# Kernel optimization log

Hardware: AMD Instinct MI355X
Metric: run time of the kernel (lower is better)

Reference implementation:

```python
import jax, jax.numpy as jnp
import numpy as np

BS, NC, C, D = 8, 64, 256, 32
K, KB, ALPHA, B = 16, 8, 4, 16
HS, HM, HMOD = 64, 64, 32
N = NC * C
DLM = NC * D
MOD_IN = K + 3 * D + 1    # 113
MOD_OUT = K + KB + 1 + D  # 57


def setup_inputs() -> dict:
    key = jax.random.key(0)
    ks = jax.random.split(key, 12)
    rn = lambda k, s, sc=1.0: jax.random.normal(k, s, dtype=jnp.float32) * sc
    s_in, m_in = 3 * D + 1, 3 * D
    inp = {}
    inp['cc_signals_t'] = rn(ks[0], (BS, DLM))
    inp['h'] = rn(ks[1], (BS, NC, C, D), 0.1)
    inp['prev_messages'] = rn(ks[2], (BS, NC, C, D), 0.1)
    inp['decay_logit'] = jnp.zeros((BS, NC, C), jnp.float32)
    inp['primitives_state'] = jnp.zeros((BS, NC, C, D), jnp.float32)
    inp['hebbian_traces'] = jnp.zeros((BS, NC, C, K), jnp.float32)
    inp['state_w1'] = rn(ks[3], (HS, s_in), (2.0 / (s_in + HS)) ** 0.5)
    inp['state_b1'] = jnp.zeros((HS,), jnp.float32)
    inp['state_w2'] = rn(ks[4], (D, HS), (2.0 / (HS + D)) ** 0.5)
    inp['state_b2'] = jnp.zeros((D,), jnp.float32)
    inp['msg_w1'] = rn(ks[5], (HM, m_in), (2.0 / (m_in + HM)) ** 0.5)
    inp['msg_b1'] = jnp.zeros((HM,), jnp.float32)
    inp['msg_w2'] = rn(ks[6], (D, HM), (2.0 / (HM + D)) ** 0.5)
    inp['msg_b2'] = jnp.zeros((D,), jnp.float32)
    inp['mod_w1'] = rn(ks[7], (N, HMOD, MOD_IN), (2.0 / (MOD_IN + HMOD)) ** 0.5)
    inp['mod_b1'] = jnp.zeros((N, HMOD), jnp.float32)
    inp['mod_w2'] = rn(ks[8], (N, HMOD, MOD_OUT), (2.0 / (HMOD + MOD_OUT)) ** 0.5)
    inp['mod_b2'] = jnp.zeros((N, MOD_OUT), jnp.float32)
    inp['neuron_id'] = rn(ks[9], (NC, C, D), 1.0 / D ** 0.5)
    inp['conn_indices'] = jax.random.randint(ks[10], (NC, C, K), 0, C)
    inp['border_conn_indices'] = jax.random.randint(ks[11], (NC, B, KB), 0, NC * B)
    return inp


def reference(cc_signals_t, h, prev_messages, decay_logit, primitives_state,
              hebbian_traces, state_w1, state_b1, state_w2, state_b2,
              msg_w1, msg_b1, msg_w2, msg_b2,
              mod_w1, mod_b1, mod_w2, mod_b2, neuron_id,
              conn_indices, border_conn_indices):
    # ---- per-neuron modulator: each of N=NC*C neurons has unique MLP weights ----
    nid = jnp.broadcast_to(neuron_id[None], (BS, NC, C, D))
    mod_inp = jnp.concatenate(
        [hebbian_traces, h, decay_logit[..., None], primitives_state, nid], axis=-1)
    flat = mod_inp.reshape(BS, N, MOD_IN)
    hid = jnp.tanh(jnp.einsum('bni,nhi->bnh', flat, mod_w1) + mod_b1)
    out = (jnp.einsum('bnh,nho->bno', hid, mod_w2) + mod_b2).reshape(BS, NC, C, MOD_OUT)
    new_w_conn = out[..., :K]                          # [BS,NC,C,K]
    w_border = out[:, :, ALPHA:ALPHA + B, K:K + KB]    # border neurons only [BS,NC,B,KB]
    new_decay = out[..., K + KB]                       # [BS,NC,C]
    new_prim = out[..., K + KB + 1:]                   # [BS,NC,C,D]

    # ---- intra-cell weighted neighbor gather (irregular gather) ----
    cell = jnp.arange(NC)[:, None, None]
    neighbor = prev_messages[:, cell, conn_indices]    # [BS,NC,C,K,D]
    received = jnp.einsum('bnckd,bnck->bncd', neighbor, jax.nn.sigmoid(new_w_conn))

    # ---- inter-cell border gather over global border neuron pool ----
    border_msgs = prev_messages[:, :, ALPHA:ALPHA + B, :].reshape(BS, NC * B, D)
    nb = border_msgs[:, border_conn_indices]           # [BS,NC,B,KB,D]
    recv_border = jnp.einsum('bnjkd,bnjk->bnjd', nb, jax.nn.sigmoid(w_border))
    received = received.at[:, :, ALPHA:ALPHA + B, :].add(recv_border)

    # ---- inject external signal into the first ALPHA neurons of each cell ----
    inj = cc_signals_t.reshape(BS, NC, 1, D)
    received = received.at[:, :, :ALPHA, :].add(
        jnp.broadcast_to(inj, (BS, NC, ALPHA, D)))

    # ---- decay-gated state update through shared state MLP ----
    primitives_new = primitives_state + new_prim
    decay = jax.nn.sigmoid(new_decay)[..., None]       # [BS,NC,C,1]
    s_in = jnp.concatenate([h, received, primitives_new, decay], axis=-1)  # 3D+1
    sh = jnp.tanh(jnp.einsum('...i,hi->...h', s_in, state_w1) + state_b1)
    dh = jnp.einsum('...h,dh->...d', sh, state_w2) + state_b2
    h_new = decay * h + (1.0 - decay) * jnp.tanh(dh)

    # ---- shared message MLP ----
    m_in = jnp.concatenate([h_new, received, nid], axis=-1)  # 3D
    mh = jnp.tanh(jnp.einsum('...i,hi->...h', m_in, msg_w1) + msg_b1)
    msg = jnp.tanh(jnp.einsum('...h,dh->...d', mh, msg_w2) + msg_b2)

    # ---- hebbian trace EMA: pre/post message correlation per connection ----
    nb_new = msg[:, cell, conn_indices]                # [BS,NC,C,K,D]
    corr = jnp.einsum('bncd,bnckd->bnck', msg, nb_new) / D
    hebbian_new = 0.9 * hebbian_traces + 0.1 * corr

    # ---- readout: mean over last ALPHA (readout) neurons per cell ----
    readout = msg[:, :, C - ALPHA:, :].mean(axis=2).reshape(BS, DLM)
    return readout, h_new, msg, hebbian_new
```

## Files before the change

### kernel.cpp

```cpp
#include <hip/hip_runtime.h>
#include <cstdint>
#include <cstddef>

constexpr int kBS = 8;
constexpr int kNC = 64;
constexpr int kC = 256;
constexpr int kD = 32;
constexpr int kK = 16;
constexpr int kKB = 8;
constexpr int kALPHA = 4;
constexpr int kB = 16;
constexpr int kHS = 64;
constexpr int kHM = 64;
constexpr int kHMOD = 32;
constexpr int kN = kNC * kC;
constexpr int kMODIN = kK + 3 * kD + 1;
constexpr int kMODOUT = kK + kKB + 1 + kD;
constexpr int kXS = 116;
constexpr int kW1S = 100;
constexpr int kSLAB = 36;

constexpr size_t kO1 = (size_t)kBS * kNC * kD;
constexpr size_t kO2 = kO1 + (size_t)kBS * kN * kD;
constexpr size_t kO3 = kO2 + (size_t)kBS * kN * kD;

__device__ __forceinline__ float sigmoidf_(float x) {
    return 1.0f / (1.0f + __expf(-x));
}
__device__ __forceinline__ float rdlane(float v, int l) {
    return __int_as_float(__builtin_amdgcn_readlane(__float_as_int(v), l));
}

__global__ __launch_bounds__(256) void mod_mlp_kernel(
    const float* __restrict__ heb, const float* __restrict__ h,
    const float* __restrict__ dlog, const float* __restrict__ prim,
    const float* __restrict__ nid,
    const float* __restrict__ mw1, const float* __restrict__ mb1,
    const float* __restrict__ mw2, const float* __restrict__ mb2,
    float* __restrict__ modout, int mos, int poff)
{
    const int wv = threadIdx.x >> 6;
    const int lane = threadIdx.x & 63;
    const int n = (blockIdx.x << 2) | wv;

    __shared__ __align__(16) float xs[4][kBS * kXS];
    float* xw = xs[wv];

    for (int t = lane; t < kBS * kMODIN; t += 64) {
        int b = t / kMODIN;
        int i = t - b * kMODIN;
        size_t nb = (size_t)b * kN + n;
        float v;
        if (i < kK)                 v = heb[nb * kK + i];
        else if (i < kK + kD)       v = h[nb * kD + (i - kK)];
        else if (i == kK + kD)      v = dlog[nb];
        else if (i < kK + 2*kD + 1) v = prim[nb * kD + (i - (kK + kD + 1))];
        else                        v = nid[(size_t)n * kD + (i - (kK + 2*kD + 1))];
        xw[b * kXS + i] = v;
    }
    __syncthreads();

    const int hh = lane & 31;
    const int bh = lane >> 5;
    const float* wg = mw1 + ((size_t)n * kHMOD + hh) * kMODIN;
    float a0 = 0.f, a1 = 0.f, a2 = 0.f, a3 = 0.f;
    #pragma unroll 4
    for (int q = 0; q < 28; ++q) {
        float w0 = wg[4*q+0], w1 = wg[4*q+1], w2 = wg[4*q+2], w3 = wg[4*q+3];
        const float4 x0 = *(const float4*)(xw + (bh+0) * kXS + 4*q);
        const float4 x1 = *(const float4*)(xw + (bh+2) * kXS + 4*q);
        const float4 x2 = *(const float4*)(xw + (bh+4) * kXS + 4*q);
        const float4 x3 = *(const float4*)(xw + (bh+6) * kXS + 4*q);
        a0 += w0*x0.x + w1*x0.y + w2*x0.z + w3*x0.w;
        a1 += w0*x1.x + w1*x1.y + w2*x1.z + w3*x1.w;
        a2 += w0*x2.x + w1*x2.y + w2*x2.z + w3*x2.w;
        a3 += w0*x3.x + w1*x3.y + w2*x3.z + w3*x3.w;
    }
    {
        float w112 = wg[112];
        a0 += w112 * xw[(bh+0)*kXS + 112];
        a1 += w112 * xw[(bh+2)*kXS + 112];
        a2 += w112 * xw[(bh+4)*kXS + 112];
        a3 += w112 * xw[(bh+6)*kXS + 112];
    }
    const float bb = mb1[(size_t)n * kHMOD + hh];
    float h0 = tanhf(a0 + bb);
    float h1 = tanhf(a1 + bb);
    float h2 = tanhf(a2 + bb);
    float h3 = tanhf(a3 + bb);

    const int o = (lane < kMODOUT) ? lane : (kMODOUT - 1);
    const float* w2g = mw2 + (size_t)n * (kHMOD * kMODOUT);
    float ob0=0.f, ob1=0.f, ob2=0.f, ob3=0.f, ob4=0.f, ob5=0.f, ob6=0.f, ob7=0.f;
    #pragma unroll
    for (int hx = 0; hx < kHMOD; ++hx) {
        float w = w2g[hx * kMODOUT + o];
        ob0 += rdlane(h0, hx)      * w;
        ob1 += rdlane(h0, hx + 32) * w;
        ob2 += rdlane(h1, hx)      * w;
        ob3 += rdlane(h1, hx + 32) * w;
        ob4 += rdlane(h2, hx)      * w;
        ob5 += rdlane(h2, hx + 32) * w;
        ob6 += rdlane(h3, hx)      * w;
        ob7 += rdlane(h3, hx + 32) * w;
    }
    if (lane < kMODOUT) {
        const float bo = mb2[(size_t)n * kMODOUT + o];
        const int oo = (o < 25) ? o : (o + (poff - 25));
        modout[((size_t)0 * kN + n) * mos + oo] = ob0 + bo;
        modout[((size_t)1 * kN + n) * mos + oo] = ob1 + bo;
        modout[((size_t)2 * kN + n) * mos + oo] = ob2 + bo;
        modout[((size_t)3 * kN + n) * mos + oo] = ob3 + bo;
        modout[((size_t)4 * kN + n) * mos + oo] = ob4 + bo;
        modout[((size_t)5 * kN + n) * mos + oo] = ob5 + bo;
        modout[((size_t)6 * kN + n) * mos + oo] = ob6 + bo;
        modout[((size_t)7 * kN + n) * mos + oo] = ob7 + bo;
    }
}

__global__ __launch_bounds__(256) void cell_kernel(
    const float* __restrict__ cc, const float* __restrict__ hin,
    const float* __restrict__ pmsg, const float* __restrict__ prim,
    const float* __restrict__ hebin, const float* __restrict__ nid,
    const float* __restrict__ sw1, const float* __restrict__ sb1,
    const float* __restrict__ sw2, const float* __restrict__ sb2,
    const float* __restrict__ mw1g, const float* __restrict__ mb1g,
    const float* __restrict__ mw2g, const float* __restrict__ mb2g,
    const int* __restrict__ conn, const int* __restrict__ bconn,
    const float* __restrict__ modout, float* __restrict__ out,
    int mos, int poff)
{
    const int nc = blockIdx.x;
    const int b  = blockIdx.y;
    const int c  = threadIdx.x;

    __shared__ __align__(16) float slab[kC * kSLAB];
    __shared__ __align__(16) float w1s[kHS * kW1S];
    __shared__ __align__(16) float w2ts[kHS * kD];
    __shared__ __align__(16) float mw1s[kHM * 96];
    __shared__ __align__(16) float mw2ts[kHM * kD];
    __shared__ float sb1s[kHS], sb2s[kD], mb1s[kHM], mb2s[kD];

    const size_t cellrow = ((size_t)b * kNC + nc) * kC;
    const size_t nbase   = cellrow + c;

    for (int idx = c; idx < kHS * 97; idx += kC) {
        int r = idx / 97, ci = idx - r * 97;
        w1s[r * kW1S + ci] = sw1[idx];
    }
    for (int idx = c; idx < kHM * 96; idx += kC) mw1s[idx] = mw1g[idx];
    for (int idx = c; idx < kHS * kD; idx += kC) {
        int o2 = idx >> 6, h2 = idx & 63;
        w2ts[h2 * kD + o2] = sw2[idx];
    }
    for (int idx = c; idx < kHM * kD; idx += kC) {
        int o2 = idx >> 6, h2 = idx & 63;
        mw2ts[h2 * kD + o2] = mw2g[idx];
    }
    if (c < kHS) sb1s[c] = sb1[c];
    if (c < kD)  sb2s[c] = sb2[c];
    if (c < kHM) mb1s[c] = mb1g[c];
    if (c < kD)  mb2s[c] = mb2g[c];

    {
        const float4* s4 = (const float4*)(pmsg + cellrow * kD);
        for (int i = c; i < (kC * kD) / 4; i += kC) {
            float4 v = s4[i];
            *(float4*)&slab[(i >> 3) * kSLAB + ((i & 7) << 2)] = v;
        }
    }

    float hreg[32];
    {
        const float4* src = (const float4*)(hin + nbase * kD);
        #pragma unroll
        for (int q = 0; q < 8; ++q) {
            float4 v = src[q];
            hreg[4*q] = v.x; hreg[4*q+1] = v.y; hreg[4*q+2] = v.z; hreg[4*q+3] = v.w;
        }
    }
    const float* mo = modout + nbase * mos;
    float wcon[16];
    if (poff == 28) {
        const float4* m4 = (const float4*)mo;
        float4 va = m4[0], vb = m4[1], vc = m4[2], vd = m4[3];
        wcon[0]=sigmoidf_(va.x);  wcon[1]=sigmoidf_(va.y);  wcon[2]=sigmoidf_(va.z);  wcon[3]=sigmoidf_(va.w);
        wcon[4]=sigmoidf_(vb.x);  wcon[5]=sigmoidf_(vb.y);  wcon[6]=sigmoidf_(vb.z);  wcon[7]=sigmoidf_(vb.w);
        wcon[8]=sigmoidf_(vc.x);  wcon[9]=sigmoidf_(vc.y);  wcon[10]=sigmoidf_(vc.z); wcon[11]=sigmoidf_(vc.w);
        wcon[12]=sigmoidf_(vd.x); wcon[13]=sigmoidf_(vd.y); wcon[14]=sigmoidf_(vd.z); wcon[15]=sigmoidf_(vd.w);
    } else {
        #pragma unroll
        for (int k = 0; k < 16; ++k) wcon[k] = sigmoidf_(mo[k]);
    }
    int jreg[16];
    {
        const int4* cr = (const int4*)(conn + ((size_t)nc * kC + c) * kK);
        #pragma unroll
        for (int q = 0; q < 4; ++q) {
            int4 v = cr[q];
            jreg[4*q] = v.x; jreg[4*q+1] = v.y; jreg[4*q+2] = v.z; jreg[4*q+3] = v.w;
        }
    }
    const float decay = sigmoidf_(mo[kK + kKB]);
    float pnew[32];
    {
        const float4* p4 = (const float4*)(prim + nbase * kD);
        if (poff == 28) {
            const float4* d4 = (const float4*)(mo + 28);
            #pragma unroll
            for (int q = 0; q < 8; ++q) {
                float4 v = p4[q], w = d4[q];
                pnew[4*q]   = v.x + w.x;
                pnew[4*q+1] = v.y + w.y;
                pnew[4*q+2] = v.z + w.z;
                pnew[4*q+3] = v.w + w.w;
            }
        } else {
            #pragma unroll
            for (int q = 0; q < 8; ++q) {
                float4 v = p4[q];
                pnew[4*q]   = v.x + mo[25 + 4*q];
                pnew[4*q+1] = v.y + mo[25 + 4*q + 1];
                pnew[4*q+2] = v.z + mo[25 + 4*q + 2];
                pnew[4*q+3] = v.w + mo[25 + 4*q + 3];
            }
        }
    }
    __syncthreads();

    float recv[32];
    #pragma unroll
    for (int d = 0; d < 32; ++d) recv[d] = 0.f;
    #pragma unroll 1
    for (int k = 0; k < 16; ++k) {
        const float4* row = (const float4*)(slab + jreg[k] * kSLAB);
        const float w = wcon[k];
        #pragma unroll
        for (int q = 0; q < 8; ++q) {
            float4 v = row[q];
            recv[4*q]   += v.x * w;
            recv[4*q+1] += v.y * w;
            recv[4*q+2] += v.z * w;
            recv[4*q+3] += v.w * w;
        }
    }
    if (c >= kALPHA && c < kALPHA + kB) {
        const int j = c - kALPHA;
        const int* br = bconn + ((size_t)nc * kB + j) * kKB;
        #pragma unroll 1
        for (int kb = 0; kb < kKB; ++kb) {
            int g = br[kb];
            int nc2 = g >> 4;
            int c2 = kALPHA + (g & 15);
            const float4* src = (const float4*)(pmsg + (((size_t)b * kNC + nc2) * kC + c2) * kD);
            float w = sigmoidf_(mo[kK + kb]);
            #pragma unroll
            for (int q = 0; q < 8; ++q) {
                float4 v = src[q];
                recv[4*q]   += v.x * w;
                recv[4*q+1] += v.y * w;
                recv[4*q+2] += v.z * w;
                recv[4*q+3] += v.w * w;
            }
        }
    }
    if (c < kALPHA) {
        const float* src = cc + (size_t)b * (kNC * kD) + nc * kD;
        #pragma unroll
        for (int d = 0; d < 32; ++d) recv[d] += src[d];
    }

    float dh[32];
    #pragma unroll
    for (int o = 0; o < 32; ++o) dh[o] = sb2s[o];
    #pragma unroll 2
    for (int hh = 0; hh < kHS; ++hh) {
        const float4* w4 = (const float4*)(w1s + hh * kW1S);
        float p0 = 0.f, p1 = 0.f, p2 = 0.f, p3 = 0.f;
        #pragma unroll
        for (int q = 0; q < 8; ++q) {
            float4 wv = w4[q];
            p0 += hreg[4*q] * wv.x;   p1 += hreg[4*q+1] * wv.y;
            p2 += hreg[4*q+2] * wv.z; p3 += hreg[4*q+3] * wv.w;
        }
        #pragma unroll
        for (int q = 0; q < 8; ++q) {
            float4 wv = w4[8+q];
            p0 += recv[4*q] * wv.x;   p1 += recv[4*q+1] * wv.y;
            p2 += recv[4*q+2] * wv.z; p3 += recv[4*q+3] * wv.w;
        }
        #pragma unroll
        for (int q = 0; q < 8; ++q) {
            float4 wv = w4[16+q];
            p0 += pnew[4*q] * wv.x;   p1 += pnew[4*q+1] * wv.y;
            p2 += pnew[4*q+2] * wv.z; p3 += pnew[4*q+3] * wv.w;
        }
        float acc = sb1s[hh] + ((p0 + p1) + (p2 + p3)) + decay * w1s[hh * kW1S + 96];
        const float s = tanhf(acc);
        const float4* w2r = (const float4*)(w2ts + hh * kD);
        #pragma unroll
        for (int q = 0; q < 8; ++q) {
            float4 wv = w2r[q];
            dh[4*q]   += s * wv.x;
            dh[4*q+1] += s * wv.y;
            dh[4*q+2] += s * wv.z;
            dh[4*q+3] += s * wv.w;
        }
    }
    float hnew[32];
    #pragma unroll
    for (int d = 0; d < 32; ++d) hnew[d] = decay * hreg[d] + (1.f - decay) * tanhf(dh[d]);

    {
        float4* dst = (float4*)(out + kO1 + nbase * kD);
        #pragma unroll
        for (int q = 0; q < 8; ++q)
            dst[q] = make_float4(hnew[4*q], hnew[4*q+1], hnew[4*q+2], hnew[4*q+3]);
    }

    float nidr[32];
    {
        const float4* src = (const float4*)(nid + ((size_t)nc * kC + c) * kD);
        #pragma unroll
        for (int q = 0; q < 8; ++q) {
            float4 v = src[q];
            nidr[4*q] = v.x; nidr[4*q+1] = v.y; nidr[4*q+2] = v.z; nidr[4*q+3] = v.w;
        }
    }
    float mm[32];
    #pragma unroll
    for (int o = 0; o < 32; ++o) mm[o] = mb2s[o];
    #pragma unroll 2
    for (int hh = 0; hh < kHM; ++hh) {
        const float4* w4 = (const float4*)(mw1s + hh * 96);
        float p0 = 0.f, p1 = 0.f, p2 = 0.f, p3 = 0.f;
        #pragma unroll
        for (int q = 0; q < 8; ++q) {
            float4 wv = w4[q];
            p0 += hnew[4*q] * wv.x;   p1 += hnew[4*q+1] * wv.y;
            p2 += hnew[4*q+2] * wv.z; p3 += hnew[4*q+3] * wv.w;
        }
        #pragma unroll
        for (int q = 0; q < 8; ++q) {
            float4 wv = w4[8+q];
            p0 += recv[4*q] * wv.x;   p1 += recv[4*q+1] * wv.y;
            p2 += recv[4*q+2] * wv.z; p3 += recv[4*q+3] * wv.w;
        }
        #pragma unroll
        for (int q = 0; q < 8; ++q) {
            float4 wv = w4[16+q];
            p0 += nidr[4*q] * wv.x;   p1 += nidr[4*q+1] * wv.y;
            p2 += nidr[4*q+2] * wv.z; p3 += nidr[4*q+3] * wv.w;
        }
        const float s = tanhf(mb1s[hh] + ((p0 + p1) + (p2 + p3)));
        const float4* w2r = (const float4*)(mw2ts + hh * kD);
        #pragma unroll
        for (int q = 0; q < 8; ++q) {
            float4 wv = w2r[q];
            mm[4*q]   += s * wv.x;
            mm[4*q+1] += s * wv.y;
            mm[4*q+2] += s * wv.z;
            mm[4*q+3] += s * wv.w;
        }
    }
    float msgr[32];
    #pragma unroll
    for (int d = 0; d < 32; ++d) msgr[d] = tanhf(mm[d]);

    __syncthreads();
    {
        float4* row = (float4*)(slab + c * kSLAB);
        #pragma unroll
        for (int q = 0; q < 8; ++q)
            row[q] = make_float4(msgr[4*q], msgr[4*q+1], msgr[4*q+2], msgr[4*q+3]);
    }
    __syncthreads();

    {
        const float* hb = hebin + nbase * kK;
        float* dst = out + kO3 + nbase * kK;
        #pragma unroll 1
        for (int k = 0; k < 16; ++k) {
            const float4* row = (const float4*)(slab + jreg[k] * kSLAB);
            float dot = 0.f;
            #pragma unroll
            for (int q = 0; q < 8; ++q) {
                float4 v = row[q];
                dot += msgr[4*q] * v.x + msgr[4*q+1] * v.y
                     + msgr[4*q+2] * v.z + msgr[4*q+3] * v.w;
            }
            dst[k] = 0.9f * hb[k] + 0.1f * (dot * (1.0f / 32.0f));
        }
    }
    {
        float4* dst = (float4*)(out + kO2 + cellrow * kD);
        for (int i = c; i < (kC * kD) / 4; i += kC)
            dst[i] = *(const float4*)&slab[(i >> 3) * kSLAB + ((i & 7) << 2)];
    }
    if (c < kD) {
        float s = 0.25f * (slab[(kC-4)*kSLAB + c] + slab[(kC-3)*kSLAB + c] +
                           slab[(kC-2)*kSLAB + c] + slab[(kC-1)*kSLAB + c]);
        out[(size_t)b * (kNC * kD) + nc * kD + c] = s;
    }
}

extern "C" void kernel_launch(void* const* d_in, const int* in_sizes, int n_in,
                              void* d_out, int out_size, void* d_ws, size_t ws_size,
                              hipStream_t stream)
{
    const float* cc    = (const float*)d_in[0];
    const float* h     = (const float*)d_in[1];
    const float* pmsg  = (const float*)d_in[2];
    const float* dlog  = (const float*)d_in[3];
    const float* prim  = (const float*)d_in[4];
    const float* heb   = (const float*)d_in[5];
    const float* sw1   = (const float*)d_in[6];
    const float* sb1   = (const float*)d_in[7];
    const float* sw2   = (const float*)d_in[8];
    const float* sb2   = (const float*)d_in[9];
    const float* mw1   = (const float*)d_in[10];
    const float* mb1   = (const float*)d_in[11];
    const float* mw2   = (const float*)d_in[12];
    const float* mb2   = (const float*)d_in[13];
    const float* modw1 = (const float*)d_in[14];
    const float* modb1 = (const float*)d_in[15];
    const float* modw2 = (const float*)d_in[16];
    const float* modb2 = (const float*)d_in[17];
    const float* nid   = (const float*)d_in[18];
    const int*   conn  = (const int*)d_in[19];
    const int*   bconn = (const int*)d_in[20];
    float* out = (float*)d_out;
    float* modout = (float*)d_ws;

    int mos = 57, poff = 25;
    if (ws_size >= (size_t)kBS * kN * 60 * sizeof(float)) { mos = 60; poff = 28; }

    mod_mlp_kernel<<<kN / 4, 256, 0, stream>>>(heb, h, dlog, prim, nid,
                                               modw1, modb1, modw2, modb2,
                                               modout, mos, poff);
    cell_kernel<<<dim3(kNC, kBS), kC, 0, stream>>>(cc, h, pmsg, prim, heb, nid,
                                                   sw1, sb1, sw2, sb2,
                                                   mw1, mb1, mw2, mb2,
                                                   conn, bconn, modout, out,
                                                   mos, poff);
}
```

Before: 766.1 us.

## Restructure mod MLP to one neuron per block; read shared-MLP W1 from global

The per-neuron modulator kernel now gives each neuron a whole 256-thread block. It stages that neuron's W1 and W2 in LDS with coalesced float4 loads, computes the hidden layer one (batch, hidden) pair per thread, and runs the output layer from LDS instead of using cross-lane readlane broadcasts. The cell kernel stops staging the shared state and message W1 matrices and biases in LDS and reads them from global or scalar memory with uniform addresses. It also pads the transposed W2 tiles and removes the vectorized modout loads for the padded layout. This cuts LDS footprint and setup cost, but the mod kernel launches four times as many blocks, and the cell kernel's inner loops now depend on global or constant-cache weight loads.

```diff
diff --git a/kernel.cpp b/kernel.cpp
--- a/kernel.cpp
+++ b/kernel.cpp
@@ -17,8 +17,9 @@
 constexpr int kMODIN = kK + 3 * kD + 1;
 constexpr int kMODOUT = kK + kKB + 1 + kD;
 constexpr int kXS = 116;
-constexpr int kW1S = 100;
+constexpr int kWS = 116;
 constexpr int kSLAB = 36;
+constexpr int kW2TS = 36;
 
 constexpr size_t kO1 = (size_t)kBS * kNC * kD;
 constexpr size_t kO2 = kO1 + (size_t)kBS * kN * kD;
@@ -26,9 +27,6 @@
 
 __device__ __forceinline__ float sigmoidf_(float x) {
     return 1.0f / (1.0f + __expf(-x));
-}
-__device__ __forceinline__ float rdlane(float v, int l) {
-    return __int_as_float(__builtin_amdgcn_readlane(__float_as_int(v), l));
 }
 
 __global__ __launch_bounds__(256) void mod_mlp_kernel(
@@ -39,82 +37,85 @@
     const float* __restrict__ mw2, const float* __restrict__ mb2,
     float* __restrict__ modout, int mos, int poff)
 {
-    const int wv = threadIdx.x >> 6;
-    const int lane = threadIdx.x & 63;
-    const int n = (blockIdx.x << 2) | wv;
-
-    __shared__ __align__(16) float xs[4][kBS * kXS];
-    float* xw = xs[wv];
-
-    for (int t = lane; t < kBS * kMODIN; t += 64) {
-        int b = t / kMODIN;
-        int i = t - b * kMODIN;
-        size_t nb = (size_t)b * kN + n;
-        float v;
-        if (i < kK)                 v = heb[nb * kK + i];
-        else if (i < kK + kD)       v = h[nb * kD + (i - kK)];
-        else if (i == kK + kD)      v = dlog[nb];
-        else if (i < kK + 2*kD + 1) v = prim[nb * kD + (i - (kK + kD + 1))];
-        else                        v = nid[(size_t)n * kD + (i - (kK + 2*kD + 1))];
-        xw[b * kXS + i] = v;
-    }
-    __syncthreads();
-
-    const int hh = lane & 31;
-    const int bh = lane >> 5;
-    const float* wg = mw1 + ((size_t)n * kHMOD + hh) * kMODIN;
-    float a0 = 0.f, a1 = 0.f, a2 = 0.f, a3 = 0.f;
-    #pragma unroll 4
-    for (int q = 0; q < 28; ++q) {
-        float w0 = wg[4*q+0], w1 = wg[4*q+1], w2 = wg[4*q+2], w3 = wg[4*q+3];
-        const float4 x0 = *(const float4*)(xw + (bh+0) * kXS + 4*q);
-        const float4 x1 = *(const float4*)(xw + (bh+2) * kXS + 4*q);
-        const float4 x2 = *(const float4*)(xw + (bh+4) * kXS + 4*q);
-        const float4 x3 = *(const float4*)(xw + (bh+6) * kXS + 4*q);
-        a0 += w0*x0.x + w1*x0.y + w2*x0.z + w3*x0.w;
-        a1 += w0*x1.x + w1*x1.y + w2*x1.z + w3*x1.w;
-        a2 += w0*x2.x + w1*x2.y + w2*x2.z + w3*x2.w;
-        a3 += w0*x3.x + w1*x3.y + w2*x3.z + w3*x3.w;
-    }
-    {
-        float w112 = wg[112];
-        a0 += w112 * xw[(bh+0)*kXS + 112];
-        a1 += w112 * xw[(bh+2)*kXS + 112];
-        a2 += w112 * xw[(bh+4)*kXS + 112];
-        a3 += w112 * xw[(bh+6)*kXS + 112];
-    }
-    const float bb = mb1[(size_t)n * kHMOD + hh];
-    float h0 = tanhf(a0 + bb);
-    float h1 = tanhf(a1 + bb);
-    float h2 = tanhf(a2 + bb);
-    float h3 = tanhf(a3 + bb);
-
-    const int o = (lane < kMODOUT) ? lane : (kMODOUT - 1);
-    const float* w2g = mw2 + (size_t)n * (kHMOD * kMODOUT);
-    float ob0=0.f, ob1=0.f, ob2=0.f, ob3=0.f, ob4=0.f, ob5=0.f, ob6=0.f, ob7=0.f;
-    #pragma unroll
-    for (int hx = 0; hx < kHMOD; ++hx) {
-        float w = w2g[hx * kMODOUT + o];
-        ob0 += rdlane(h0, hx)      * w;
-        ob1 += rdlane(h0, hx + 32) * w;
-        ob2 += rdlane(h1, hx)      * w;
-        ob3 += rdlane(h1, hx + 32) * w;
-        ob4 += rdlane(h2, hx)      * w;
-        ob5 += rdlane(h2, hx + 32) * w;
-        ob6 += rdlane(h3, hx)      * w;
-        ob7 += rdlane(h3, hx + 32) * w;
-    }
-    if (lane < kMODOUT) {
-        const float bo = mb2[(size_t)n * kMODOUT + o];
-        const int oo = (o < 25) ? o : (o + (poff - 25));
-        modout[((size_t)0 * kN + n) * mos + oo] = ob0 + bo;
-        modout[((size_t)1 * kN + n) * mos + oo] = ob1 + bo;
-        modout[((size_t)2 * kN + n) * mos + oo] = ob2 + bo;
-        modout[((size_t)3 * kN + n) * mos + oo] = ob3 + bo;
-        modout[((size_t)4 * kN + n) * mos + oo] = ob4 + bo;
-        modout[((size_t)5 * kN + n) * mos + oo] = ob5 + bo;
-        modout[((size_t)6 * kN + n) * mos + oo] = ob6 + bo;
-        modout[((size_t)7 * kN + n) * mos + oo] = ob7 + bo;
+    const int n = blockIdx.x;
+    const int tid = threadIdx.x;
+
+    __shared__ __align__(16) float xw[kBS * kXS];
+    __shared__ __align__(16) float w1s[kHMOD * kWS];
+    __shared__ __align__(16) float w2s[kHMOD * kMODOUT];
+    __shared__ float hids[kBS * kHMOD];
+
+    {
+        const float4* w1g4 = (const float4*)(mw1 + (size_t)n * (kHMOD * kMODIN));
+        #pragma unroll
+        for (int r = 0; r < 4; ++r) {
+            int t = tid + 256 * r;
+            if (t < (kHMOD * kMODIN) / 4) {
+                float4 v = w1g4[t];
+                int f = t << 2;
+                #pragma unroll
+                for (int e = 0; e < 4; ++e) {
+                    int fe = f + e;
+                    int row = fe / kMODIN;
+                    int col = fe - row * kMODIN;
+                    float val = (e == 0) ? v.x : (e == 1) ? v.y : (e == 2) ? v.z : v.w;
+                    w1s[row * kWS + col] = val;
+                }
+            }
+        }
+    }
+    {
+        const float4* w2g4 = (const float4*)(mw2 + (size_t)n * (kHMOD * kMODOUT));
+        #pragma unroll
+        for (int r = 0; r < 2; ++r) {
+            int t = tid + 256 * r;
+            if (t < (kHMOD * kMODOUT) / 4)
+                *(float4*)&w2s[t << 2] = w2g4[t];
+        }
+    }
+    {
+        if (tid < kBS * kK) {
+            int b = tid >> 4, i = tid & 15;
+            xw[b * kXS + i] = heb[((size_t)b * kN + n) * kK + i];
+        }
+        {
+            int b = tid >> 5, d = tid & 31;
+            xw[b * kXS + 16 + d] = h[((size_t)b * kN + n) * kD + d];
+            xw[b * kXS + 49 + d] = prim[((size_t)b * kN + n) * kD + d];
+            xw[b * kXS + 81 + d] = nid[(size_t)n * kD + d];
+        }
+        if (tid < kBS)
+            xw[tid * kXS + 48] = dlog[(size_t)tid * kN + n];
+    }
+    __syncthreads();
+
+    {
+        const int hh = tid & 31;
+        const int b  = tid >> 5;
+        const float* wr = w1s + hh * kWS;
+        const float* xr = xw + b * kXS;
+        float acc = mb1[(size_t)n * kHMOD + hh];
+        #pragma unroll 4
+        for (int q = 0; q < 28; ++q) {
+            float4 wv = *(const float4*)(wr + 4*q);
+            float4 xv = *(const float4*)(xr + 4*q);
+            acc += wv.x*xv.x + wv.y*xv.y + wv.z*xv.z + wv.w*xv.w;
+        }
+        acc += wr[112] * xr[112];
+        hids[b * kHMOD + hh] = tanhf(acc);
+    }
+    __syncthreads();
+
+    for (int t = tid; t < kBS * kMODOUT; t += 256) {
+        int b2 = t / kMODOUT;
+        int o  = t - b2 * kMODOUT;
+        const float* hr = hids + b2 * kHMOD;
+        float acc = mb2[(size_t)n * kMODOUT + o];
+        #pragma unroll
+        for (int hx = 0; hx < kHMOD; ++hx)
+            acc += hr[hx] * w2s[hx * kMODOUT + o];
+        int oo = (o < 25) ? o : (o + (poff - 25));
+        modout[((size_t)b2 * kN + n) * mos + oo] = acc;
     }
 }
 
@@ -135,32 +136,20 @@
     const int c  = threadIdx.x;
 
     __shared__ __align__(16) float slab[kC * kSLAB];
-    __shared__ __align__(16) float w1s[kHS * kW1S];
-    __shared__ __align__(16) float w2ts[kHS * kD];
-    __shared__ __align__(16) float mw1s[kHM * 96];
-    __shared__ __align__(16) float mw2ts[kHM * kD];
-    __shared__ float sb1s[kHS], sb2s[kD], mb1s[kHM], mb2s[kD];
+    __shared__ __align__(16) float w2ts[kHS * kW2TS];
+    __shared__ __align__(16) float mw2ts[kHM * kW2TS];
 
     const size_t cellrow = ((size_t)b * kNC + nc) * kC;
     const size_t nbase   = cellrow + c;
 
-    for (int idx = c; idx < kHS * 97; idx += kC) {
-        int r = idx / 97, ci = idx - r * 97;
-        w1s[r * kW1S + ci] = sw1[idx];
-    }
-    for (int idx = c; idx < kHM * 96; idx += kC) mw1s[idx] = mw1g[idx];
     for (int idx = c; idx < kHS * kD; idx += kC) {
         int o2 = idx >> 6, h2 = idx & 63;
-        w2ts[h2 * kD + o2] = sw2[idx];
+        w2ts[h2 * kW2TS + o2] = sw2[idx];
     }
     for (int idx = c; idx < kHM * kD; idx += kC) {
         int o2 = idx >> 6, h2 = idx & 63;
-        mw2ts[h2 * kD + o2] = mw2g[idx];
-    }
-    if (c < kHS) sb1s[c] = sb1[c];
-    if (c < kD)  sb2s[c] = sb2[c];
-    if (c < kHM) mb1s[c] = mb1g[c];
-    if (c < kD)  mb2s[c] = mb2g[c];
+        mw2ts[h2 * kW2TS + o2] = mw2g[idx];
+    }
 
     {
         const float4* s4 = (const float4*)(pmsg + cellrow * kD);
@@ -181,17 +170,8 @@
     }
     const float* mo = modout + nbase * mos;
     float wcon[16];
-    if (poff == 28) {
-        const float4* m4 = (const float4*)mo;
-        float4 va = m4[0], vb = m4[1], vc = m4[2], vd = m4[3];
-        wcon[0]=sigmoidf_(va.x);  wcon[1]=sigmoidf_(va.y);  wcon[2]=sigmoidf_(va.z);  wcon[3]=sigmoidf_(va.w);
-        wcon[4]=sigmoidf_(vb.x);  wcon[5]=sigmoidf_(vb.y);  wcon[6]=sigmoidf_(vb.z);  wcon[7]=sigmoidf_(vb.w);
-        wcon[8]=sigmoidf_(vc.x);  wcon[9]=sigmoidf_(vc.y);  wcon[10]=sigmoidf_(vc.z); wcon[11]=sigmoidf_(vc.w);
-        wcon[12]=sigmoidf_(vd.x); wcon[13]=sigmoidf_(vd.y); wcon[14]=sigmoidf_(vd.z); wcon[15]=sigmoidf_(vd.w);
-    } else {
-        #pragma unroll
-        for (int k = 0; k < 16; ++k) wcon[k] = sigmoidf_(mo[k]);
-    }
+    #pragma unroll
+    for (int k = 0; k < 16; ++k) wcon[k] = sigmoidf_(mo[k]);
     int jreg[16];
     {
         const int4* cr = (const int4*)(conn + ((size_t)nc * kC + c) * kK);
@@ -205,25 +185,14 @@
     float pnew[32];
     {
         const float4* p4 = (const float4*)(prim + nbase * kD);
-        if (poff == 28) {
-            const float4* d4 = (const float4*)(mo + 28);
-            #pragma unroll
-            for (int q = 0; q < 8; ++q) {
-                float4 v = p4[q], w = d4[q];
-                pnew[4*q]   = v.x + w.x;
-                pnew[4*q+1] = v.y + w.y;
-                pnew[4*q+2] = v.z + w.z;
-                pnew[4*q+3] = v.w + w.w;
-            }
-        } else {
-            #pragma unroll
-            for (int q = 0; q < 8; ++q) {
-                float4 v = p4[q];
-                pnew[4*q]   = v.x + mo[25 + 4*q];
-                pnew[4*q+1] = v.y + mo[25 + 4*q + 1];
-                pnew[4*q+2] = v.z + mo[25 + 4*q + 2];
-                pnew[4*q+3] = v.w + mo[25 + 4*q + 3];
-            }
+        const int pbase = poff;
+        #pragma unroll
+        for (int q = 0; q < 8; ++q) {
+            float4 v = p4[q];
+            pnew[4*q]   = v.x + mo[pbase + 4*q];
+            pnew[4*q+1] = v.y + mo[pbase + 4*q + 1];
+            pnew[4*q+2] = v.z + mo[pbase + 4*q + 2];
+            pnew[4*q+3] = v.w + mo[pbase + 4*q + 3];
         }
     }
     __syncthreads();
@@ -272,32 +241,19 @@
 
     float dh[32];
     #pragma unroll
-    for (int o = 0; o < 32; ++o) dh[o] = sb2s[o];
+    for (int o = 0; o < 32; ++o) dh[o] = sb2[o];
     #pragma unroll 2
     for (int hh = 0; hh < kHS; ++hh) {
-        const float4* w4 = (const float4*)(w1s + hh * kW1S);
-        float p0 = 0.f, p1 = 0.f, p2 = 0.f, p3 = 0.f;
-        #pragma unroll
-        for (int q = 0; q < 8; ++q) {
-            float4 wv = w4[q];
-            p0 += hreg[4*q] * wv.x;   p1 += hreg[4*q+1] * wv.y;
-            p2 += hreg[4*q+2] * wv.z; p3 += hreg[4*q+3] * wv.w;
-        }
-        #pragma unroll
-        for (int q = 0; q < 8; ++q) {
-            float4 wv = w4[8+q];
-            p0 += recv[4*q] * wv.x;   p1 += recv[4*q+1] * wv.y;
-            p2 += recv[4*q+2] * wv.z; p3 += recv[4*q+3] * wv.w;
-        }
-        #pragma unroll
-        for (int q = 0; q < 8; ++q) {
-            float4 wv = w4[16+q];
-            p0 += pnew[4*q] * wv.x;   p1 += pnew[4*q+1] * wv.y;
-            p2 += pnew[4*q+2] * wv.z; p3 += pnew[4*q+3] * wv.w;
-        }
-        float acc = sb1s[hh] + ((p0 + p1) + (p2 + p3)) + decay * w1s[hh * kW1S + 96];
+        const float* w = sw1 + hh * (3 * kD + 1);
+        float acc = sb1[hh] + decay * w[96];
+        #pragma unroll
+        for (int i = 0; i < 32; ++i) acc += hreg[i] * w[i];
+        #pragma unroll
+        for (int i = 0; i < 32; ++i) acc += recv[i] * w[32 + i];
+        #pragma unroll
+        for (int i = 0; i < 32; ++i) acc += pnew[i] * w[64 + i];
         const float s = tanhf(acc);
-        const float4* w2r = (const float4*)(w2ts + hh * kD);
+        const float4* w2r = (const float4*)(w2ts + hh * kW2TS);
         #pragma unroll
         for (int q = 0; q < 8; ++q) {
             float4 wv = w2r[q];
@@ -329,31 +285,19 @@
     }
     float mm[32];
     #pragma unroll
-    for (int o = 0; o < 32; ++o) mm[o] = mb2s[o];
+    for (int o = 0; o < 32; ++o) mm[o] = mb2g[o];
     #pragma unroll 2
     for (int hh = 0; hh < kHM; ++hh) {
-        const float4* w4 = (const float4*)(mw1s + hh * 96);
-        float p0 = 0.f, p1 = 0.f, p2 = 0.f, p3 = 0.f;
-        #pragma unroll
-        for (int q = 0; q < 8; ++q) {
-            float4 wv = w4[q];
-            p0 += hnew[4*q] * wv.x;   p1 += hnew[4*q+1] * wv.y;
-            p2 += hnew[4*q+2] * wv.z; p3 += hnew[4*q+3] * wv.w;
-        }
-        #pragma unroll
-        for (int q = 0; q < 8; ++q) {
-            float4 wv = w4[8+q];
-            p0 += recv[4*q] * wv.x;   p1 += recv[4*q+1] * wv.y;
-            p2 += recv[4*q+2] * wv.z; p3 += recv[4*q+3] * wv.w;
-        }
-        #pragma unroll
-        for (int q = 0; q < 8; ++q) {
-            float4 wv = w4[16+q];
-            p0 += nidr[4*q] * wv.x;   p1 += nidr[4*q+1] * wv.y;
-            p2 += nidr[4*q+2] * wv.z; p3 += nidr[4*q+3] * wv.w;
-        }
-        const float s = tanhf(mb1s[hh] + ((p0 + p1) + (p2 + p3)));
-        const float4* w2r = (const float4*)(mw2ts + hh * kD);
+        const float* w = mw1g + hh * (3 * kD);
+        float acc = mb1g[hh];
+        #pragma unroll
+        for (int i = 0; i < 32; ++i) acc += hnew[i] * w[i];
+        #pragma unroll
+        for (int i = 0; i < 32; ++i) acc += recv[i] * w[32 + i];
+        #pragma unroll
+        for (int i = 0; i < 32; ++i) acc += nidr[i] * w[64 + i];
+        const float s = tanhf(acc);
+        const float4* w2r = (const float4*)(mw2ts + hh * kW2TS);
         #pragma unroll
         for (int q = 0; q < 8; ++q) {
             float4 wv = w2r[q];
@@ -435,9 +379,9 @@
     int mos = 57, poff = 25;
     if (ws_size >= (size_t)kBS * kN * 60 * sizeof(float)) { mos = 60; poff = 28; }
 
-    mod_mlp_kernel<<<kN / 4, 256, 0, stream>>>(heb, h, dlog, prim, nid,
-                                               modw1, modb1, modw2, modb2,
-                                               modout, mos, poff);
+    mod_mlp_kernel<<<kN, 256, 0, stream>>>(heb, h, dlog, prim, nid,
+                                           modw1, modb1, modw2, modb2,
+                                           modout, mos, poff);
     cell_kernel<<<dim3(kNC, kBS), kC, 0, stream>>>(cc, h, pmsg, prim, heb, nid,
                                                    sw1, sb1, sw2, sb2,
                                                    mw1, mb1, mw2, mb2,
```

Result: faster. 729.1 us (-4.8%).
